# Kernel optimization log

Measured on AMD Instinct MI355X. Metric: run time of the kernel, lower is better.

Reference implementation:

```python
import jax, jax.numpy as jnp
import numpy as np

B, NPG, DEG = 32, 1024, 16          # graphs, nodes/graph, avg degree
N, E = B * NPG, B * NPG * DEG        # 32768 nodes, 524288 edges
IN_C, HID, H, EDGE_D = 128, 64, 4, 8
RATIO = 0.5
K = int(np.ceil(RATIO * NPG))        # 512 nodes kept per graph (static)
SLOPE = 0.2                          # PyG GATConv LeakyReLU default


def setup_inputs() -> dict:
    key = jax.random.key(0)
    ks = jax.random.split(key, 10)
    x = jax.random.normal(ks[0], (N, IN_C), jnp.float32)
    # edges confined within each graph (block structure like PyG Batch)
    src_l = jax.random.randint(ks[1], (B, NPG * DEG), 0, NPG)
    dst_l = jax.random.randint(ks[2], (B, NPG * DEG), 0, NPG)
    off = (jnp.arange(B) * NPG)[:, None]
    edge_index = jnp.stack([(src_l + off).reshape(-1), (dst_l + off).reshape(-1)]).astype(jnp.int64)
    edge = jax.random.normal(ks[3], (E, EDGE_D), jnp.float32)
    batch_index = jnp.repeat(jnp.arange(B), NPG).astype(jnp.int64)
    s_in = 1.0 / np.sqrt(IN_C)
    W = jax.random.normal(ks[4], (IN_C, H, HID), jnp.float32) * s_in
    a_src = jax.random.normal(ks[5], (H, HID), jnp.float32) * s_in
    a_dst = jax.random.normal(ks[6], (H, HID), jnp.float32) * s_in
    b_gat = jnp.zeros((H * HID,), jnp.float32)
    W_lin = jax.random.normal(ks[7], (H * HID, HID), jnp.float32) * (1.0 / np.sqrt(H * HID))
    b_lin = jnp.zeros((HID,), jnp.float32)
    p_pool = jax.random.normal(ks[8], (HID,), jnp.float32)
    return dict(x=x, edge_index=edge_index, edge=edge, batch_index=batch_index,
                W=W, a_src=a_src, a_dst=a_dst, b_gat=b_gat,
                W_lin=W_lin, b_lin=b_lin, p_pool=p_pool)


def reference(x, edge_index, edge, batch_index, W, a_src, a_dst, b_gat, W_lin, b_lin, p_pool):
    n = x.shape[0]
    # --- GATConv (heads concat, self-loops added, softmax over incoming edges) ---
    loops = jnp.arange(n)
    src = jnp.concatenate([edge_index[0], loops])
    dst = jnp.concatenate([edge_index[1], loops])
    h = jnp.einsum('ni,ihc->nhc', x, W)                  # [N,H,C]
    al_src = (h * a_src).sum(-1)                          # [N,H]
    al_dst = (h * a_dst).sum(-1)                          # [N,H]
    e = jax.nn.leaky_relu(al_src[src] + al_dst[dst], SLOPE)  # [Etot,H]
    m = jax.ops.segment_max(e, dst, num_segments=n)
    ex = jnp.exp(e - m[dst])
    denom = jax.ops.segment_sum(ex, dst, num_segments=n)
    alpha = ex / denom[dst]                               # segment softmax per target
    out = jax.ops.segment_sum(h[src] * alpha[:, :, None], dst, num_segments=n)
    xg = out.reshape(n, H * HID) + b_gat
    # --- Linear ---
    xl = xg @ W_lin + b_lin                               # [N,HID]
    # --- TopKPooling (tanh(x.p/||p||) score, top ceil(ratio*n) per graph) ---
    score = jnp.tanh(xl @ p_pool / jnp.linalg.norm(p_pool))   # [N]
    topv, topi = jax.lax.top_k(score.reshape(B, NPG), K)      # [B,K]
    perm = (topi + (jnp.arange(B) * NPG)[:, None]).reshape(-1)  # global kept node ids
    xp = xl[perm] * topv.reshape(-1)[:, None]             # [B*K,HID], gated by score
    batch_out = jnp.repeat(jnp.arange(B), K)
    # edge filtering / remapping (padded with -1 instead of compacting)
    nmap = jnp.full((n,), -1, jnp.int32).at[perm].set(jnp.arange(B * K, dtype=jnp.int32))
    ns, nd = nmap[edge_index[0]], nmap[edge_index[1]]
    valid = (ns >= 0) & (nd >= 0)
    edge_index_new = jnp.where(valid, jnp.stack([ns, nd]), -1)
    edge_new = jnp.where(valid[:, None], edge, 0.0)
    # --- global mean/max pool (graphs are contiguous blocks of K nodes) ---
    xr = xp.reshape(B, K, HID)
    x1 = jnp.concatenate([xr.mean(axis=1), xr.max(axis=1)], axis=-1)  # [B,2*HID]
    return xp, edge_index_new, edge_new, batch_out, x1
```

## Files before the change

### kernel.cpp

```cpp
#include <hip/hip_runtime.h>
#include <math.h>

#define NN   32768
#define EE   524288
#define ETOT (EE + NN)
#define BB   32
#define NPG  1024
#define EPG  16384
#define RPG  17408
#define KK   512
#define INC  128
#define HID  64
#define NH   4
#define CC   256
#define SLOPE 0.2f

typedef __attribute__((ext_vector_type(8))) short short8;
typedef __attribute__((ext_vector_type(4))) float f32x4;

static __device__ inline unsigned short f2bf(float f) {
  unsigned u = __float_as_uint(f);
  unsigned r = (u + 0x7FFFu + ((u >> 16) & 1u)) >> 16;
  return (unsigned short)r;
}

__global__ __launch_bounds__(256) void prep_kernel(const float* __restrict__ W,
                                                   const float* __restrict__ a_src,
                                                   const float* __restrict__ a_dst,
                                                   const float* __restrict__ b_gat,
                                                   const float* __restrict__ W_lin,
                                                   const float* __restrict__ b_lin,
                                                   const float* __restrict__ p,
                                                   float* __restrict__ Mg,
                                                   float* __restrict__ cbuf,
                                                   unsigned short* __restrict__ Wt,
                                                   unsigned short* __restrict__ Wlt) {
  const int b = blockIdx.x, t = threadIdx.x;
  if (b >= 17) {
    int idx = (b - 17) * 256 + t;
    if (idx < 32768) {
      int c = idx >> 7, k = idx & 127;
      Wt[idx] = f2bf(W[k * 256 + c]);
    } else {
      int i2 = idx - 32768;
      int c = i2 >> 8, k = i2 & 255;
      Wlt[i2] = f2bf(W_lin[k * 64 + c]);
    }
    return;
  }
  __shared__ float pl[64];
  __shared__ float ql[256];
  __shared__ float red[256];
  __shared__ float red2[256];
  if (t < 64) pl[t] = p[t];
  __syncthreads();
  {
    float acc = 0.f;
    const float* wr = W_lin + t * 64;
#pragma unroll
    for (int c = 0; c < 64; c += 4) {
      float4 wv = *(const float4*)(wr + c);
      acc += wv.x * pl[c] + wv.y * pl[c + 1] + wv.z * pl[c + 2] + wv.w * pl[c + 3];
    }
    ql[t] = acc;
  }
  __syncthreads();
  if (b == 0) {
    float r = ql[t] * b_gat[t];
    if (t < 64) r += b_lin[t] * pl[t];
    red[t] = r;
    red2[t] = (t < 64) ? pl[t] * pl[t] : 0.f;
    __syncthreads();
    for (int s2 = 128; s2 > 0; s2 >>= 1) {
      if (t < s2) { red[t] += red[t + s2]; red2[t] += red2[t + s2]; }
      __syncthreads();
    }
    if (t == 0) { cbuf[0] = red[0]; cbuf[1] = 1.0f / sqrtf(red2[0]); }
    return;
  }
  if (t < 96) {
    const int i = (b - 1) * 8 + t / 12;
    const int j = t % 12;
    const int hh = j & 3;
    const float* wr = W + i * 256 + hh * 64;
    float acc = 0.f;
    if (j < 8) {
      const float* v = (j < 4 ? a_src : a_dst) + hh * 64;
#pragma unroll
      for (int c = 0; c < 64; c += 4) {
        float4 wv = *(const float4*)(wr + c);
        float4 vv = *(const float4*)(v + c);
        acc += wv.x * vv.x + wv.y * vv.y + wv.z * vv.z + wv.w * vv.w;
      }
    } else {
#pragma unroll
      for (int c = 0; c < 64; ++c) acc += wr[c] * ql[hh * 64 + c];
    }
    Mg[i * 12 + j] = acc;
  }
}

__global__ __launch_bounds__(256) void prep_node_kernel(const float* __restrict__ x,
                                                        const float* __restrict__ Mg,
                                                        float* __restrict__ al_s,
                                                        float* __restrict__ al_d,
                                                        float* __restrict__ hq) {
  __shared__ float xs[64][132];
  __shared__ float MsT[12][132];
  const int t = threadIdx.x;
  const int n0 = blockIdx.x * 64;
  for (int r = t; r < 1536; r += 256) MsT[r % 12][r / 12] = Mg[r];
#pragma unroll
  for (int u = 0; u < 8; ++u) {
    int idx = u * 256 + t;
    int node = idx >> 5, c4 = idx & 31;
    *(float4*)(&xs[node][c4 * 4]) =
        *(const float4*)(x + (size_t)(n0 + node) * 128 + c4 * 4);
  }
  __syncthreads();
  const int node = t >> 2, q = t & 3;
  const int j0 = q * 3;
  float a0 = 0.f, a1 = 0.f, a2 = 0.f;
#pragma unroll
  for (int c4 = 0; c4 < 32; ++c4) {
    float4 xv = *(const float4*)(&xs[node][c4 * 4]);
    float4 m0 = *(const float4*)(&MsT[j0 + 0][c4 * 4]);
    float4 m1 = *(const float4*)(&MsT[j0 + 1][c4 * 4]);
    float4 m2 = *(const float4*)(&MsT[j0 + 2][c4 * 4]);
    a0 += xv.x * m0.x + xv.y * m0.y + xv.z * m0.z + xv.w * m0.w;
    a1 += xv.x * m1.x + xv.y * m1.y + xv.z * m1.z + xv.w * m1.w;
    a2 += xv.x * m2.x + xv.y * m2.y + xv.z * m2.z + xv.w * m2.w;
  }
  const int n = n0 + node;
  float vals[3] = {a0, a1, a2};
#pragma unroll
  for (int k = 0; k < 3; ++k) {
    int j = j0 + k;
    float* base = (j < 4) ? al_s : ((j < 8) ? al_d : hq);
    int jj = (j < 4) ? j : ((j < 8) ? j - 4 : j - 8);
    base[n * 4 + jj] = vals[k];
  }
}

__global__ __launch_bounds__(256) void gemm1_kernel(const float* __restrict__ x,
                                                    const unsigned short* __restrict__ Wt,
                                                    unsigned short* __restrict__ hbf) {
  const int lane = threadIdx.x & 63;
  const int wv = threadIdx.x >> 6;
  const int q = lane >> 4, nh = lane & 15;
  const int lid = blockIdx.x;
  const int node = ((lid & 7) * 64 + (lid >> 3)) * 64 + wv * 16 + nh;
  f32x4 acc[16];
#pragma unroll
  for (int mt = 0; mt < 16; ++mt) acc[mt] = (f32x4){0.f, 0.f, 0.f, 0.f};
  const float* xr = x + (size_t)node * 128;
#pragma unroll
  for (int kc = 0; kc < 4; ++kc) {
    const float* xp = xr + kc * 32 + q * 8;
    float4 v0 = *(const float4*)(xp);
    float4 v1 = *(const float4*)(xp + 4);
    short8 b;
    b[0] = (short)f2bf(v0.x); b[1] = (short)f2bf(v0.y);
    b[2] = (short)f2bf(v0.z); b[3] = (short)f2bf(v0.w);
    b[4] = (short)f2bf(v1.x); b[5] = (short)f2bf(v1.y);
    b[6] = (short)f2bf(v1.z); b[7] = (short)f2bf(v1.w);
#pragma unroll
    for (int mt = 0; mt < 16; ++mt) {
      short8 a = *(const short8*)(Wt + (size_t)(mt * 16 + nh) * 128 + kc * 32 + q * 8);
      acc[mt] = __builtin_amdgcn_mfma_f32_16x16x32_bf16(a, b, acc[mt], 0, 0, 0);
    }
  }
  unsigned short* hr = hbf + (size_t)node * 256;
#pragma unroll
  for (int mt = 0; mt < 16; ++mt) {
    ushort4 o;
    o.x = f2bf(acc[mt][0]); o.y = f2bf(acc[mt][1]);
    o.z = f2bf(acc[mt][2]); o.w = f2bf(acc[mt][3]);
    *(ushort4*)(hr + mt * 16 + q * 4) = o;
  }
}

__global__ __launch_bounds__(1024) void scan_scatter_kernel(const int* __restrict__ ei,
                                                            int* __restrict__ row_ptr,
                                                            int* __restrict__ col) {
  __shared__ int hist[NPG];
  __shared__ int lpos[NPG];
  __shared__ int wsum[16];
  const int b = blockIdx.x, t = threadIdx.x;
  const int lane = t & 63, wid = t >> 6;
  hist[t] = 0;
  __syncthreads();
  const int e0 = b * EPG;
  for (int k = t; k < EPG; k += 1024)
    atomicAdd(&hist[ei[EE + e0 + k] - b * NPG], 1);
  __syncthreads();
  const int c = hist[t] + 1;
  int inc = c;
#pragma unroll
  for (int off = 1; off < 64; off <<= 1) {
    int u = __shfl_up(inc, off, 64);
    if (lane >= off) inc += u;
  }
  if (lane == 63) wsum[wid] = inc;
  __syncthreads();
  if (wid == 0) {
    int v = (lane < 16) ? wsum[lane] : 0;
#pragma unroll
    for (int off = 1; off < 16; off <<= 1) {
      int u = __shfl_up(v, off, 64);
      if (lane >= off) v += u;
    }
    if (lane < 16) wsum[lane] = v;
  }
  __syncthreads();
  const int woff = (wid == 0) ? 0 : wsum[wid - 1];
  const int excl = woff + inc - c;
  row_ptr[b * NPG + t] = b * RPG + excl;
  lpos[t] = excl;
  if (b == 0 && t == 0) row_ptr[NN] = ETOT;
  __syncthreads();
  {
    int p0 = atomicAdd(&lpos[t], 1);
    col[b * RPG + p0] = b * NPG + t;
  }
  for (int k = t; k < EPG; k += 1024) {
    int s = ei[e0 + k];
    int d = ei[EE + e0 + k];
    int p1 = atomicAdd(&lpos[d - b * NPG], 1);
    col[b * RPG + p1] = s;
  }
}

__global__ __launch_bounds__(256) void agg_kernel(const unsigned short* __restrict__ h,
                                                  const float* __restrict__ al_s,
                                                  const float* __restrict__ al_d,
                                                  const float* __restrict__ hq,
                                                  const int* __restrict__ row_ptr,
                                                  const int* __restrict__ col,
                                                  const float* __restrict__ b_gat,
                                                  const float* __restrict__ cbuf,
                                                  unsigned short* __restrict__ outg,
                                                  float* __restrict__ score) {
  __shared__ float wsh[4][256];
  __shared__ float qsh[4][256];
  __shared__ int   osh[4][64];
  const int lane = threadIdx.x & 63;
  const int wv = threadIdx.x >> 6;
  const int hqi = lane >> 4;
  const int xcd = blockIdx.x & 7;
  const int jb = blockIdx.x >> 3;
  const int n = (xcd * 1024 + jb) * 4 + wv;
  const int beg = row_ptr[n], end = row_ptr[n + 1];
  const float4 ad4 = *(const float4*)(al_d + (size_t)n * 4);
  const char* hbase = (const char*)h + (size_t)lane * 8;
  float ax = 0.f, ay = 0.f, az = 0.f, aw = 0.f, den = 0.f, sq = 0.f;
  for (int base = beg; base < end; base += 64) {
    const int rem = end - base;
    const int cnt = rem < 64 ? rem : 64;
    if (lane < cnt) {
      const int c = col[base + lane];
      osh[wv][lane] = c << 9;
      const float4 as = *(const float4*)(al_s + (size_t)c * 4);
      float e0 = as.x + ad4.x; e0 = (e0 > 0.f) ? e0 : SLOPE * e0;
      float e1 = as.y + ad4.y; e1 = (e1 > 0.f) ? e1 : SLOPE * e1;
      float e2 = as.z + ad4.z; e2 = (e2 > 0.f) ? e2 : SLOPE * e2;
      float e3 = as.w + ad4.w; e3 = (e3 > 0.f) ? e3 : SLOPE * e3;
      *(float4*)(&wsh[wv][lane * 4]) =
          make_float4(__expf(e0), __expf(e1), __expf(e2), __expf(e3));
      *(float4*)(&qsh[wv][lane * 4]) = *(const float4*)(hq + (size_t)c * 4);
    }
    const int cm1 = cnt - 1;
    uint2 v0 = *(const uint2*)(hbase + osh[wv][0]);
    uint2 v1 = *(const uint2*)(hbase + osh[wv][1 > cm1 ? cm1 : 1]);
    uint2 v2 = *(const uint2*)(hbase + osh[wv][2 > cm1 ? cm1 : 2]);
    uint2 v3 = *(const uint2*)(hbase + osh[wv][3 > cm1 ? cm1 : 3]);
    for (int i = 0; i < cnt; ++i) {
      const float w = wsh[wv][i * 4 + hqi];
      const float hqv = qsh[wv][i * 4 + hqi];
      uint2 cur = v0; v0 = v1; v1 = v2; v2 = v3;
      int ni = i + 4; ni = ni > cm1 ? cm1 : ni;
      v3 = *(const uint2*)(hbase + osh[wv][ni]);
      den += w; sq += w * hqv;
      ax += w * __uint_as_float(cur.x << 16);
      ay += w * __uint_as_float(cur.x & 0xffff0000u);
      az += w * __uint_as_float(cur.y << 16);
      aw += w * __uint_as_float(cur.y & 0xffff0000u);
    }
  }
  const float4 bg = *(const float4*)(b_gat + lane * 4);
  ushort4 ov;
  ov.x = f2bf(ax / den + bg.x); ov.y = f2bf(ay / den + bg.y);
  ov.z = f2bf(az / den + bg.z); ov.w = f2bf(aw / den + bg.w);
  *(ushort4*)(outg + (size_t)n * 256 + lane * 4) = ov;
  float sd = sq / den;
  float s0v = __shfl(sd, 0), s1v = __shfl(sd, 16);
  float s2v = __shfl(sd, 32), s3v = __shfl(sd, 48);
  if (lane == 0)
    score[n] = tanhf((s0v + s1v + s2v + s3v + cbuf[0]) * cbuf[1]);
}

__global__ __launch_bounds__(1024) void topk_kernel(const float* __restrict__ score,
                                                    int* __restrict__ pidx_g,
                                                    float* __restrict__ tvs_g,
                                                    int* __restrict__ nmap,
                                                    float* __restrict__ out_batch) {
  __shared__ float scv[NPG];
  const int blk = blockIdx.x;
  const int b = blk >> 3, slice = blk & 7;
  const int t = threadIdx.x;
  scv[t] = score[b * NPG + t];
  __syncthreads();
  const int node = slice * 128 + (t >> 3);
  const int sub = t & 7;
  const float sc = scv[node];
  int rank = 0;
#pragma unroll
  for (int m = 0; m < 32; ++m) {
    const int j = (m * 8 + sub) * 4;
    const float4 s4 = *(const float4*)(&scv[j]);
    rank += (s4.x > sc) || (s4.x == sc && (j + 0) < node);
    rank += (s4.y > sc) || (s4.y == sc && (j + 1) < node);
    rank += (s4.z > sc) || (s4.z == sc && (j + 2) < node);
    rank += (s4.w > sc) || (s4.w == sc && (j + 3) < node);
  }
  rank += __shfl_xor(rank, 1, 64);
  rank += __shfl_xor(rank, 2, 64);
  rank += __shfl_xor(rank, 4, 64);
  if (sub == 0) {
    const int gn = b * NPG + node;
    if (rank < KK) {
      pidx_g[b * KK + rank] = node;
      tvs_g[b * KK + rank] = sc;
      nmap[gn] = b * KK + rank;
      out_batch[b * KK + rank] = (float)b;
    } else {
      nmap[gn] = -1;
    }
  }
}

__global__ __launch_bounds__(256) void gemm2xp_kernel(const unsigned short* __restrict__ outg,
                                                      const unsigned short* __restrict__ Wlt,
                                                      const float* __restrict__ bl,
                                                      const int* __restrict__ pidx_g,
                                                      const float* __restrict__ tvs_g,
                                                      float* __restrict__ out_xp) {
  const int lane = threadIdx.x & 63, wv = threadIdx.x >> 6;
  const int q = lane >> 4, nh = lane & 15;
  const int g = blockIdx.x >> 3, o = blockIdx.x & 7;
  const int r = o * 64 + wv * 16 + nh;
  const int gnode = g * NPG + pidx_g[g * KK + r];
  const float tv = tvs_g[g * KK + r];
  f32x4 acc[4];
#pragma unroll
  for (int mt = 0; mt < 4; ++mt) acc[mt] = (f32x4){0.f, 0.f, 0.f, 0.f};
  const unsigned short* ar = outg + (size_t)gnode * 256;
#pragma unroll
  for (int kc = 0; kc < 8; ++kc) {
    short8 bf = *(const short8*)(ar + kc * 32 + q * 8);
#pragma unroll
    for (int mt = 0; mt < 4; ++mt) {
      short8 a = *(const short8*)(Wlt + (size_t)(mt * 16 + nh) * 256 + kc * 32 + q * 8);
      acc[mt] = __builtin_amdgcn_mfma_f32_16x16x32_bf16(a, bf, acc[mt], 0, 0, 0);
    }
  }
#pragma unroll
  for (int mt = 0; mt < 4; ++mt) {
    const int c4 = mt * 16 + q * 4;
    float4 bl4 = *(const float4*)(bl + c4);
    float4 o4 = make_float4((acc[mt][0] + bl4.x) * tv, (acc[mt][1] + bl4.y) * tv,
                            (acc[mt][2] + bl4.z) * tv, (acc[mt][3] + bl4.w) * tv);
    *(float4*)(out_xp + (size_t)(g * KK + r) * HID + c4) = o4;
  }
}

__global__ __launch_bounds__(1024) void pool_kernel(const float* __restrict__ out_xp,
                                                    float* __restrict__ out_x1) {
  __shared__ float ps[16][64];
  __shared__ float pm[16][64];
  const int b = blockIdx.x, t = threadIdx.x;
  const int c = t & 63, rg = t >> 6;
  float s = 0.f, m = -INFINITY;
  for (int row = rg; row < KK; row += 16) {
    float vv = out_xp[(size_t)(b * KK + row) * HID + c];
    s += vv; m = fmaxf(m, vv);
  }
  ps[rg][c] = s; pm[rg][c] = m;
  __syncthreads();
  if (t < 64) {
    float st = 0.f, mt = -INFINITY;
#pragma unroll
    for (int g2 = 0; g2 < 16; ++g2) { st += ps[g2][t]; mt = fmaxf(mt, pm[g2][t]); }
    out_x1[b * 128 + t] = st * (1.0f / KK);
    out_x1[b * 128 + 64 + t] = mt;
  }
}

__global__ void edge_out_kernel(const int* __restrict__ ei, const float* __restrict__ edge,
                                const int* __restrict__ nmap,
                                float* __restrict__ out_ei, float* __restrict__ out_edge) {
  int e = blockIdx.x * 256 + threadIdx.x;
  if (e >= EE) return;
  int s = ei[e], d = ei[EE + e];
  int ns = nmap[s], nd = nmap[d];
  bool valid = (ns >= 0) && (nd >= 0);
  out_ei[e] = (float)(valid ? ns : -1);
  out_ei[EE + e] = (float)(valid ? nd : -1);
  const float4* ef = (const float4*)(edge + (size_t)e * 8);
  float4 z = make_float4(0.f, 0.f, 0.f, 0.f);
  float4 v0 = valid ? ef[0] : z;
  float4 v1 = valid ? ef[1] : z;
  float4* eo = (float4*)(out_edge + (size_t)e * 8);
  eo[0] = v0; eo[1] = v1;
}

extern "C" void kernel_launch(void* const* d_in, const int* in_sizes, int n_in,
                              void* d_out, int out_size, void* d_ws, size_t ws_size,
                              hipStream_t stream) {
  const float* x      = (const float*)d_in[0];
  const int*   ei     = (const int*)d_in[1];
  const float* edge   = (const float*)d_in[2];
  const float* W      = (const float*)d_in[4];
  const float* a_src  = (const float*)d_in[5];
  const float* a_dst  = (const float*)d_in[6];
  const float* b_gat  = (const float*)d_in[7];
  const float* W_lin  = (const float*)d_in[8];
  const float* b_lin  = (const float*)d_in[9];
  const float* p_pool = (const float*)d_in[10];

  char* ws = (char*)d_ws;
  size_t off = 0;
  auto alloc = [&](size_t bytes) -> void* {
    void* p = ws + off;
    off += (bytes + 255) & ~(size_t)255;
    return p;
  };
  unsigned short* hbf  = (unsigned short*)alloc((size_t)NN * CC * 2);
  unsigned short* outg = (unsigned short*)alloc((size_t)NN * CC * 2);
  float* al_s    = (float*)alloc((size_t)NN * NH * 4);
  float* al_d    = (float*)alloc((size_t)NN * NH * 4);
  float* hq      = (float*)alloc((size_t)NN * NH * 4);
  float* score   = (float*)alloc((size_t)NN * 4);
  int*   row_ptr = (int*)alloc((size_t)(NN + 1) * 4);
  int*   col     = (int*)alloc((size_t)ETOT * 4);
  int*   nmap    = (int*)alloc((size_t)NN * 4);
  int*   pidx_g  = (int*)alloc((size_t)BB * KK * 4);
  float* tvs_g   = (float*)alloc((size_t)BB * KK * 4);
  unsigned short* Wt  = (unsigned short*)alloc((size_t)CC * INC * 2);
  unsigned short* Wlt = (unsigned short*)alloc((size_t)HID * CC * 2);
  float* Mg      = (float*)alloc((size_t)INC * 12 * 4);
  float* cbuf    = (float*)alloc(2 * 4);

  float* out_xp    = (float*)d_out;
  float* out_ei    = out_xp + (size_t)BB * KK * HID;
  float* out_edge  = out_ei + 2 * (size_t)EE;
  float* out_batch = out_edge + (size_t)EE * 8;
  float* out_x1    = out_batch + (size_t)BB * KK;

  prep_kernel<<<209, 256, 0, stream>>>(W, a_src, a_dst, b_gat, W_lin, b_lin,
                                       p_pool, Mg, cbuf, Wt, Wlt);
  prep_node_kernel<<<NN / 64, 256, 0, stream>>>(x, Mg, al_s, al_d, hq);
  gemm1_kernel<<<512, 256, 0, stream>>>(x, Wt, hbf);
  scan_scatter_kernel<<<BB, 1024, 0, stream>>>(ei, row_ptr, col);
  agg_kernel<<<NN / 4, 256, 0, stream>>>(hbf, al_s, al_d, hq, row_ptr, col,
                                         b_gat, cbuf, outg, score);
  topk_kernel<<<256, 1024, 0, stream>>>(score, pidx_g, tvs_g, nmap, out_batch);
  gemm2xp_kernel<<<256, 256, 0, stream>>>(outg, Wlt, b_lin, pidx_g, tvs_g, out_xp);
  pool_kernel<<<BB, 1024, 0, stream>>>(out_xp, out_x1);
  edge_out_kernel<<<(EE + 255) / 256, 256, 0, stream>>>(ei, edge, nmap, out_ei, out_edge);
}
```

Baseline: 228.9 us.

## Merge node prep with gemm1 and fold pooling into gemm2 and edge kernels

The per-node attention-logit prep and the bf16 MFMA projection now run in a single launch, with block index selecting the role. Each gemm2 block reduces its 64-row output tile into per-block partial sums and maxima through shared memory. The first 32 blocks of the edge kernel then combine those partials into the mean/max pool. This removes two kernel launches and the re-read of the pooled output, in exchange for a larger shared-memory footprint in the merged kernel and some extra work in the gemm2 epilogue.

```diff
diff --git a/kernel.cpp b/kernel.cpp
--- a/kernel.cpp
+++ b/kernel.cpp
@@ -100,53 +100,54 @@
   }
 }
 
-__global__ __launch_bounds__(256) void prep_node_kernel(const float* __restrict__ x,
-                                                        const float* __restrict__ Mg,
-                                                        float* __restrict__ al_s,
-                                                        float* __restrict__ al_d,
-                                                        float* __restrict__ hq) {
-  __shared__ float xs[64][132];
-  __shared__ float MsT[12][132];
+__global__ __launch_bounds__(256) void stage2_kernel(const float* __restrict__ x,
+                                                     const float* __restrict__ Mg,
+                                                     const unsigned short* __restrict__ Wt,
+                                                     float* __restrict__ al_s,
+                                                     float* __restrict__ al_d,
+                                                     float* __restrict__ hq,
+                                                     unsigned short* __restrict__ hbf) {
+  __shared__ float smem[76 * 132];
   const int t = threadIdx.x;
-  const int n0 = blockIdx.x * 64;
-  for (int r = t; r < 1536; r += 256) MsT[r % 12][r / 12] = Mg[r];
-#pragma unroll
-  for (int u = 0; u < 8; ++u) {
-    int idx = u * 256 + t;
-    int node = idx >> 5, c4 = idx & 31;
-    *(float4*)(&xs[node][c4 * 4]) =
-        *(const float4*)(x + (size_t)(n0 + node) * 128 + c4 * 4);
-  }
-  __syncthreads();
-  const int node = t >> 2, q = t & 3;
-  const int j0 = q * 3;
-  float a0 = 0.f, a1 = 0.f, a2 = 0.f;
-#pragma unroll
-  for (int c4 = 0; c4 < 32; ++c4) {
-    float4 xv = *(const float4*)(&xs[node][c4 * 4]);
-    float4 m0 = *(const float4*)(&MsT[j0 + 0][c4 * 4]);
-    float4 m1 = *(const float4*)(&MsT[j0 + 1][c4 * 4]);
-    float4 m2 = *(const float4*)(&MsT[j0 + 2][c4 * 4]);
-    a0 += xv.x * m0.x + xv.y * m0.y + xv.z * m0.z + xv.w * m0.w;
-    a1 += xv.x * m1.x + xv.y * m1.y + xv.z * m1.z + xv.w * m1.w;
-    a2 += xv.x * m2.x + xv.y * m2.y + xv.z * m2.z + xv.w * m2.w;
-  }
-  const int n = n0 + node;
-  float vals[3] = {a0, a1, a2};
-#pragma unroll
-  for (int k = 0; k < 3; ++k) {
-    int j = j0 + k;
-    float* base = (j < 4) ? al_s : ((j < 8) ? al_d : hq);
-    int jj = (j < 4) ? j : ((j < 8) ? j - 4 : j - 8);
-    base[n * 4 + jj] = vals[k];
-  }
-}
-
-__global__ __launch_bounds__(256) void gemm1_kernel(const float* __restrict__ x,
-                                                    const unsigned short* __restrict__ Wt,
-                                                    unsigned short* __restrict__ hbf) {
-  const int lane = threadIdx.x & 63;
-  const int wv = threadIdx.x >> 6;
+  if (blockIdx.x >= 512) {
+    float (*xs)[132] = (float(*)[132])smem;
+    float (*MsT)[132] = (float(*)[132])(smem + 64 * 132);
+    const int n0 = (blockIdx.x - 512) * 64;
+    for (int r = t; r < 1536; r += 256) MsT[r % 12][r / 12] = Mg[r];
+#pragma unroll
+    for (int u = 0; u < 8; ++u) {
+      int idx = u * 256 + t;
+      int node = idx >> 5, c4 = idx & 31;
+      *(float4*)(&xs[node][c4 * 4]) =
+          *(const float4*)(x + (size_t)(n0 + node) * 128 + c4 * 4);
+    }
+    __syncthreads();
+    const int node = t >> 2, q = t & 3;
+    const int j0 = q * 3;
+    float a0 = 0.f, a1 = 0.f, a2 = 0.f;
+#pragma unroll
+    for (int c4 = 0; c4 < 32; ++c4) {
+      float4 xv = *(const float4*)(&xs[node][c4 * 4]);
+      float4 m0 = *(const float4*)(&MsT[j0 + 0][c4 * 4]);
+      float4 m1 = *(const float4*)(&MsT[j0 + 1][c4 * 4]);
+      float4 m2 = *(const float4*)(&MsT[j0 + 2][c4 * 4]);
+      a0 += xv.x * m0.x + xv.y * m0.y + xv.z * m0.z + xv.w * m0.w;
+      a1 += xv.x * m1.x + xv.y * m1.y + xv.z * m1.z + xv.w * m1.w;
+      a2 += xv.x * m2.x + xv.y * m2.y + xv.z * m2.z + xv.w * m2.w;
+    }
+    const int n = n0 + node;
+    float vals[3] = {a0, a1, a2};
+#pragma unroll
+    for (int k = 0; k < 3; ++k) {
+      int j = j0 + k;
+      float* base = (j < 4) ? al_s : ((j < 8) ? al_d : hq);
+      int jj = (j < 4) ? j : ((j < 8) ? j - 4 : j - 8);
+      base[n * 4 + jj] = vals[k];
+    }
+    return;
+  }
+  const int lane = t & 63;
+  const int wv = t >> 6;
   const int q = lane >> 4, nh = lane & 15;
   const int lid = blockIdx.x;
   const int node = ((lid & 7) * 64 + (lid >> 3)) * 64 + wv * 16 + nh;
@@ -344,11 +345,18 @@
                                                       const float* __restrict__ bl,
                                                       const int* __restrict__ pidx_g,
                                                       const float* __restrict__ tvs_g,
-                                                      float* __restrict__ out_xp) {
-  const int lane = threadIdx.x & 63, wv = threadIdx.x >> 6;
+                                                      float* __restrict__ out_xp,
+                                                      float* __restrict__ psum,
+                                                      float* __restrict__ pmax) {
+  __shared__ float tile[64][68];
+  __shared__ float pr[4][64];
+  __shared__ float pmx[4][64];
+  const int t = threadIdx.x;
+  const int lane = t & 63, wv = t >> 6;
   const int q = lane >> 4, nh = lane & 15;
   const int g = blockIdx.x >> 3, o = blockIdx.x & 7;
   const int r = o * 64 + wv * 16 + nh;
+  const int row = wv * 16 + nh;
   const int gnode = g * NPG + pidx_g[g * KK + r];
   const float tv = tvs_g[g * KK + r];
   f32x4 acc[4];
@@ -371,34 +379,46 @@
     float4 o4 = make_float4((acc[mt][0] + bl4.x) * tv, (acc[mt][1] + bl4.y) * tv,
                             (acc[mt][2] + bl4.z) * tv, (acc[mt][3] + bl4.w) * tv);
     *(float4*)(out_xp + (size_t)(g * KK + r) * HID + c4) = o4;
-  }
-}
-
-__global__ __launch_bounds__(1024) void pool_kernel(const float* __restrict__ out_xp,
-                                                    float* __restrict__ out_x1) {
-  __shared__ float ps[16][64];
-  __shared__ float pm[16][64];
-  const int b = blockIdx.x, t = threadIdx.x;
-  const int c = t & 63, rg = t >> 6;
-  float s = 0.f, m = -INFINITY;
-  for (int row = rg; row < KK; row += 16) {
-    float vv = out_xp[(size_t)(b * KK + row) * HID + c];
-    s += vv; m = fmaxf(m, vv);
-  }
-  ps[rg][c] = s; pm[rg][c] = m;
+    *(float4*)(&tile[row][c4]) = o4;
+  }
+  __syncthreads();
+  {
+    const int ch = t & 63, qr = t >> 6;
+    float s = 0.f, m = -INFINITY;
+#pragma unroll
+    for (int rr = 0; rr < 16; ++rr) {
+      float v = tile[qr * 16 + rr][ch];
+      s += v; m = fmaxf(m, v);
+    }
+    pr[qr][ch] = s; pmx[qr][ch] = m;
+  }
   __syncthreads();
   if (t < 64) {
-    float st = 0.f, mt = -INFINITY;
-#pragma unroll
-    for (int g2 = 0; g2 < 16; ++g2) { st += ps[g2][t]; mt = fmaxf(mt, pm[g2][t]); }
-    out_x1[b * 128 + t] = st * (1.0f / KK);
-    out_x1[b * 128 + 64 + t] = mt;
+    float s = pr[0][t] + pr[1][t] + pr[2][t] + pr[3][t];
+    float m = fmaxf(fmaxf(pr[0][t], pr[1][t]), fmaxf(pr[2][t], pr[3][t]));
+    m = fmaxf(fmaxf(pmx[0][t], pmx[1][t]), fmaxf(pmx[2][t], pmx[3][t]));
+    psum[g * 512 + o * 64 + t] = s;
+    pmax[g * 512 + o * 64 + t] = m;
   }
 }
 
 __global__ void edge_out_kernel(const int* __restrict__ ei, const float* __restrict__ edge,
                                 const int* __restrict__ nmap,
-                                float* __restrict__ out_ei, float* __restrict__ out_edge) {
+                                const float* __restrict__ psum,
+                                const float* __restrict__ pmax,
+                                float* __restrict__ out_ei, float* __restrict__ out_edge,
+                                float* __restrict__ out_x1) {
+  if (blockIdx.x < BB && threadIdx.x < 64) {
+    const int b = blockIdx.x, t = threadIdx.x;
+    float s = 0.f, m = -INFINITY;
+#pragma unroll
+    for (int o = 0; o < 8; ++o) {
+      s += psum[b * 512 + o * 64 + t];
+      m = fmaxf(m, pmax[b * 512 + o * 64 + t]);
+    }
+    out_x1[b * 128 + t] = s * (1.0f / KK);
+    out_x1[b * 128 + 64 + t] = m;
+  }
   int e = blockIdx.x * 256 + threadIdx.x;
   if (e >= EE) return;
   int s = ei[e], d = ei[EE + e];
@@ -446,6 +466,8 @@
   int*   nmap    = (int*)alloc((size_t)NN * 4);
   int*   pidx_g  = (int*)alloc((size_t)BB * KK * 4);
   float* tvs_g   = (float*)alloc((size_t)BB * KK * 4);
+  float* psum    = (float*)alloc((size_t)BB * 8 * HID * 4);
+  float* pmax    = (float*)alloc((size_t)BB * 8 * HID * 4);
   unsigned short* Wt  = (unsigned short*)alloc((size_t)CC * INC * 2);
   unsigned short* Wlt = (unsigned short*)alloc((size_t)HID * CC * 2);
   float* Mg      = (float*)alloc((size_t)INC * 12 * 4);
@@ -459,13 +481,13 @@
 
   prep_kernel<<<209, 256, 0, stream>>>(W, a_src, a_dst, b_gat, W_lin, b_lin,
                                        p_pool, Mg, cbuf, Wt, Wlt);
-  prep_node_kernel<<<NN / 64, 256, 0, stream>>>(x, Mg, al_s, al_d, hq);
-  gemm1_kernel<<<512, 256, 0, stream>>>(x, Wt, hbf);
+  stage2_kernel<<<1024, 256, 0, stream>>>(x, Mg, Wt, al_s, al_d, hq, hbf);
   scan_scatter_kernel<<<BB, 1024, 0, stream>>>(ei, row_ptr, col);
   agg_kernel<<<NN / 4, 256, 0, stream>>>(hbf, al_s, al_d, hq, row_ptr, col,
                                          b_gat, cbuf, outg, score);
   topk_kernel<<<256, 1024, 0, stream>>>(score, pidx_g, tvs_g, nmap, out_batch);
-  gemm2xp_kernel<<<256, 256, 0, stream>>>(outg, Wlt, b_lin, pidx_g, tvs_g, out_xp);
-  pool_kernel<<<BB, 1024, 0, stream>>>(out_xp, out_x1);
-  edge_out_kernel<<<(EE + 255) / 256, 256, 0, stream>>>(ei, edge, nmap, out_ei, out_edge);
-}
+  gemm2xp_kernel<<<256, 256, 0, stream>>>(outg, Wlt, b_lin, pidx_g, tvs_g,
+                                          out_xp, psum, pmax);
+  edge_out_kernel<<<(EE + 255) / 256, 256, 0, stream>>>(ei, edge, nmap, psum, pmax,
+                                                        out_ei, out_edge, out_x1);
+}
```

New measurement: 214.5 us. 1.07x faster.
